# Kernel optimization log

Measured on AMD Instinct MI355X. Metric: run time of the kernel, lower is better.

## Reference

```python
import jax, jax.numpy as jnp
import numpy as np

DIM = 1024
HEADS = 8
DIM_HEAD = 64
INNER = HEADS * DIM_HEAD  # 512
SCALE = 8.0


def l2norm(t, eps=1e-12):
    # matches F.normalize(t, dim=-1)
    n = jnp.linalg.norm(t, axis=-1, keepdims=True)
    return t / jnp.maximum(n, eps)


def setup_inputs() -> dict:
    key = jax.random.key(0)
    ks = jax.random.split(key, 5)
    x = jax.random.normal(ks[0], (4, 2048, DIM), dtype=jnp.float32)
    # torch Linear weights are [out, in]; store transposed [in, out] for x @ W
    s = 1.0 / np.sqrt(DIM)
    Wq = jax.random.uniform(ks[1], (DIM, INNER), jnp.float32, -s, s)
    Wk = jax.random.uniform(ks[2], (DIM, INNER), jnp.float32, -s, s)
    Wv = jax.random.uniform(ks[3], (DIM, INNER), jnp.float32, -s, s)
    so = 1.0 / np.sqrt(INNER)
    Wo = jax.random.uniform(ks[4], (INNER, DIM), jnp.float32, -so, so)
    return {"x": x, "Wq": Wq, "Wk": Wk, "Wv": Wv, "Wo": Wo}


def reference(x, Wq, Wk, Wv, Wo):
    b, n, _ = x.shape
    def split_heads(t):
        return t.reshape(b, n, HEADS, DIM_HEAD).transpose(0, 2, 1, 3)  # b h n d
    q = split_heads(x @ Wq)
    k = split_heads(x @ Wk)
    v = split_heads(x @ Wv)
    # cosine-sim attention: l2-normalize q, k then fixed scale
    q = l2norm(q)
    k = l2norm(k)
    sim = jnp.einsum('bhid,bhjd->bhij', q, k) * SCALE
    causal_mask = jnp.triu(jnp.ones((n, n), dtype=bool), k=1)
    sim = jnp.where(causal_mask, jnp.finfo(sim.dtype).min, sim)
    attn = jax.nn.softmax(sim, axis=-1)
    o = jnp.einsum('bhij,bhjd->bhid', attn, v)
    o = o.transpose(0, 2, 1, 3).reshape(b, n, INNER)
    return o @ Wo
```

## Files before the change

kernel.cpp:

```cpp
#include <hip/hip_runtime.h>
#include <hip/hip_bf16.h>

typedef __attribute__((ext_vector_type(8))) __bf16 bf16x8;
typedef __attribute__((ext_vector_type(4))) __bf16 bf16x4;
typedef __attribute__((ext_vector_type(4))) float f32x4;

#define MFMA16(a, b, c) __builtin_amdgcn_mfma_f32_16x16x32_bf16(a, b, c, 0, 0, 0)

static __device__ __forceinline__ ushort f2b(float f) {
    __bf16 b = (__bf16)f;
    return __builtin_bit_cast(ushort, b);
}
static __device__ __forceinline__ bf16x8 cat44(bf16x4 a, bf16x4 b) {
    bf16x8 r;
    r[0] = a[0]; r[1] = a[1]; r[2] = a[2]; r[3] = a[3];
    r[4] = b[0]; r[5] = b[1]; r[6] = b[2]; r[7] = b[3];
    return r;
}
static __device__ __forceinline__ void gload_lds16(const ushort* g, ushort* l) {
    __builtin_amdgcn_global_load_lds(
        (const __attribute__((address_space(1))) unsigned int*)g,
        (__attribute__((address_space(3))) unsigned int*)l, 16, 0, 0);
}
static __device__ __forceinline__ float exp2_fast(float x) {
    float r;
    asm("v_exp_f32 %0, %1" : "=v"(r) : "v"(x));
    return r;
}

__global__ __launch_bounds__(256)
void prep_k(const float* __restrict__ x, ushort* __restrict__ xb,
            const float* __restrict__ Wq, const float* __restrict__ Wk,
            const float* __restrict__ Wv, const float* __restrict__ Wo,
            ushort* __restrict__ Wqkv, ushort* __restrict__ Wot) {
    const int bid = blockIdx.x;
    const int tid = threadIdx.x;
    if (bid < 8192) {
        int i = bid * 256 + tid;
        float4 v = reinterpret_cast<const float4*>(x)[i];
        ushort4 o;
        o.x = f2b(v.x); o.y = f2b(v.y); o.z = f2b(v.z); o.w = f2b(v.w);
        reinterpret_cast<ushort4*>(xb)[i] = o;
        return;
    }
    __shared__ ushort T[64][72];
    const int bb = bid - 8192;
    const int job = bb >> 7;
    const int t = bb & 127;
    const float* src; ushort* dst; int K, N;
    if (job == 0)      { src = Wq; dst = Wqkv;                       K = 1024; N = 512; }
    else if (job == 1) { src = Wk; dst = Wqkv + (size_t)512 * 1024;  K = 1024; N = 512; }
    else if (job == 2) { src = Wv; dst = Wqkv + (size_t)1024 * 1024; K = 1024; N = 512; }
    else               { src = Wo; dst = Wot;                        K = 512;  N = 1024; }
    const int tn = N >> 6;
    const int bk = t / tn, bn = t - bk * tn;
    const int k0 = bk * 64, n0 = bn * 64;
#pragma unroll
    for (int q = 0; q < 4; ++q) {
        const int lin = tid + 256 * q;
        const int kr = lin >> 4;
        const int n4 = (lin & 15) << 2;
        float4 v = *reinterpret_cast<const float4*>(&src[(size_t)(k0 + kr) * N + n0 + n4]);
        T[n4 + 0][kr] = f2b(v.x);
        T[n4 + 1][kr] = f2b(v.y);
        T[n4 + 2][kr] = f2b(v.z);
        T[n4 + 3][kr] = f2b(v.w);
    }
    __syncthreads();
#pragma unroll
    for (int s = 0; s < 2; ++s) {
        const int lin = tid + 256 * s;
        const int n = lin >> 3;
        const int kc = (lin & 7) << 3;
        ushort4 a, b;
        a.x = T[n][kc + 0]; a.y = T[n][kc + 1]; a.z = T[n][kc + 2]; a.w = T[n][kc + 3];
        b.x = T[n][kc + 4]; b.y = T[n][kc + 5]; b.z = T[n][kc + 6]; b.w = T[n][kc + 7];
        ushort* p = &dst[(size_t)(n0 + n) * K + k0 + kc];
        *reinterpret_cast<ushort4*>(p) = a;
        *reinterpret_cast<ushort4*>(p + 4) = b;
    }
}

template <int F32OUT, int ROUTE>
__global__ __launch_bounds__(256)
void gemm_tile_k(const ushort* __restrict__ A, const ushort* __restrict__ Bt,
                 void* __restrict__ C0, void* __restrict__ C1, void* __restrict__ C2,
                 int M, int N, int K, int nby) {
    __shared__ __align__(16) ushort As[128 * 64];
    __shared__ __align__(16) ushort Bs[128 * 64];
    const int tid = threadIdx.x;
    const int lane = tid & 63;
    const int w = tid >> 6;
    const int l15 = lane & 15, g = lane >> 4;
    const int wr = w >> 1, wc = w & 1;

    const int nwg = gridDim.x;
    const int cpx = nwg >> 3;
    const int bid = blockIdx.x;
    const int swz = (bid & 7) * cpx + (bid >> 3);
    const int bx = swz / nby, by = swz - bx * nby;
    const int rbase = bx * 128, cbase = by * 128;

    const int lr = lane >> 3;
    const int sc = (lane & 7) ^ lr;
    const ushort* Ap = A + (size_t)(rbase + 32 * w + lr) * K + sc * 8;
    const ushort* Bp = Bt + (size_t)(cbase + 32 * w + lr) * K + sc * 8;
    ushort* AsD = &As[(32 * w) * 64];
    ushort* BsD = &Bs[(32 * w) * 64];

    f32x4 acc[4][4];
#pragma unroll
    for (int m = 0; m < 4; ++m)
#pragma unroll
        for (int n = 0; n < 4; ++n) acc[m][n] = (f32x4){0, 0, 0, 0};

    const int nk = K >> 6;
    for (int kt = 0; kt < nk; ++kt) {
        const int k0 = kt << 6;
        if (kt) __syncthreads();
#pragma unroll
        for (int i = 0; i < 4; ++i) {
            gload_lds16(Ap + (size_t)(8 * i) * K + k0, AsD + (8 * i) * 64);
            gload_lds16(Bp + (size_t)(8 * i) * K + k0, BsD + (8 * i) * 64);
        }
        __syncthreads();
        bf16x8 af[4][2], bfr[4][2];
#pragma unroll
        for (int m = 0; m < 4; ++m) {
            const int row = 64 * wr + 16 * m + l15;
#pragma unroll
            for (int kh = 0; kh < 2; ++kh) {
                const int ch = (g + 4 * kh) ^ (l15 & 7);
                af[m][kh] = *reinterpret_cast<const bf16x8*>(&As[row * 64 + ch * 8]);
            }
        }
#pragma unroll
        for (int n = 0; n < 4; ++n) {
            const int row = 64 * wc + 16 * n + l15;
#pragma unroll
            for (int kh = 0; kh < 2; ++kh) {
                const int ch = (g + 4 * kh) ^ (l15 & 7);
                bfr[n][kh] = *reinterpret_cast<const bf16x8*>(&Bs[row * 64 + ch * 8]);
            }
        }
#pragma unroll
        for (int m = 0; m < 4; ++m)
#pragma unroll
            for (int n = 0; n < 4; ++n) {
                acc[m][n] = MFMA16(af[m][0], bfr[n][0], acc[m][n]);
                acc[m][n] = MFMA16(af[m][1], bfr[n][1], acc[m][n]);
            }
    }

    if (ROUTE) {
        const int col0 = cbase + 64 * wc;
        const int grp = col0 >> 9;
        const int co0 = col0 & 511;
        if (grp == 2) {
            const int h = co0 >> 6;
#pragma unroll
            for (int m = 0; m < 4; ++m) {
                const int row = rbase + 64 * wr + 16 * m + 4 * g;
                const int bb = row >> 11;
                const int tok = row & 2047;
#pragma unroll
                for (int n = 0; n < 4; ++n) {
                    const int d = 16 * n + l15;
                    bf16x4 wv;
#pragma unroll
                    for (int r = 0; r < 4; ++r) wv[r] = (__bf16)acc[m][n][r];
                    ushort* dst = (ushort*)C2 + (((size_t)(bb * 8 + h) * 64 + d) * 2048 + tok);
                    *reinterpret_cast<bf16x4*>(dst) = wv;
                }
            }
        } else {
            ushort* Cg = (ushort*)(grp == 0 ? C0 : C1);
#pragma unroll
            for (int m = 0; m < 4; ++m) {
                f32x4 ss = {0, 0, 0, 0};
#pragma unroll
                for (int n = 0; n < 4; ++n)
#pragma unroll
                    for (int r = 0; r < 4; ++r) ss[r] += acc[m][n][r] * acc[m][n][r];
#pragma unroll
                for (int r = 0; r < 4; ++r) {
                    float s = ss[r];
                    s += __shfl_xor(s, 1);
                    s += __shfl_xor(s, 2);
                    s += __shfl_xor(s, 4);
                    s += __shfl_xor(s, 8);
                    ss[r] = 1.0f / fmaxf(sqrtf(s), 1e-12f);
                }
                const int row = rbase + 64 * wr + 16 * m + 4 * g;
#pragma unroll
                for (int n = 0; n < 4; ++n) {
                    const int co = co0 + 16 * n + l15;
#pragma unroll
                    for (int r = 0; r < 4; ++r)
                        Cg[(size_t)(row + r) * 512 + co] = f2b(acc[m][n][r] * ss[r]);
                }
            }
        }
    } else {
#pragma unroll
        for (int m = 0; m < 4; ++m)
#pragma unroll
            for (int n = 0; n < 4; ++n) {
                const int row = rbase + 64 * wr + 16 * m + 4 * g;
                const int col = cbase + 64 * wc + 16 * n + l15;
                if (F32OUT) {
#pragma unroll
                    for (int r = 0; r < 4; ++r)
                        reinterpret_cast<float*>(C0)[(size_t)(row + r) * N + col] = acc[m][n][r];
                } else {
#pragma unroll
                    for (int r = 0; r < 4; ++r)
                        reinterpret_cast<ushort*>(C0)[(size_t)(row + r) * N + col] = f2b(acc[m][n][r]);
                }
            }
    }
}

__global__ __launch_bounds__(128, 2)
void flash_attn_k(const ushort* __restrict__ Q, const ushort* __restrict__ K,
                  const ushort* __restrict__ Vt, ushort* __restrict__ O) {
    __shared__ __align__(16) ushort Ks[64 * 64];
    __shared__ __align__(16) ushort Vs[64 * 64];
    const int tid = threadIdx.x;
    const int lane = tid & 63;
    const int wave = tid >> 6;
    const int l15 = lane & 15;
    const int g = lane >> 4;
    const int bh = blockIdx.x;
    const int b = bh >> 3, h = bh & 7;
    const int j = blockIdx.y;
    const int ytrue = (j < 16) ? j : 47 - j;
    const int wglob = ytrue * 2 + wave;
    const int c0 = wglob;
    const int c1 = 127 - wglob;
    const int q0 = c0 * 16 + l15;
    const int q1 = c1 * 16 + l15;
    const int nt0 = (c0 * 16 + 79) >> 6;
    const int nt1 = (c1 * 16 + 79) >> 6;
    const int ntb = ((127 - 2 * ytrue) * 16 + 79) >> 6;

    const float CEXP = 11.5415603f;

    const ushort* Qb = Q + (size_t)(b * 2048) * 512 + h * 64;
    const ushort* Kb = K + (size_t)(b * 2048) * 512 + h * 64;
    const ushort* Vb = Vt + (size_t)bh * 64 * 2048;

    const ushort* kSrc[4];
    const ushort* vSrc[4];
    ushort* kDst[4];
    ushort* vDst[4];
#pragma unroll
    for (int i = 0; i < 4; ++i) {
        const int s = tid + 128 * i;
        const int row = s >> 3;
        const int cc = s & 7;
        const int scc = cc ^ (row & 7);
        kSrc[i] = Kb + (size_t)row * 512 + scc * 8;
        vSrc[i] = Vb + (size_t)row * 2048 + scc * 8;
        const int base = (wave * 64 + 128 * i) * 8;
        kDst[i] = &Ks[base];
        vDst[i] = &Vs[base];
    }

    bf16x8 qf0[2], qf1[2];
#pragma unroll
    for (int kh = 0; kh < 2; ++kh) {
        qf0[kh] = *reinterpret_cast<const bf16x8*>(Qb + (size_t)q0 * 512 + 32 * kh + 8 * g);
        qf1[kh] = *reinterpret_cast<const bf16x8*>(Qb + (size_t)q1 * 512 + 32 * kh + 8 * g);
    }

    bf16x8 ones;
#pragma unroll
    for (int i = 0; i < 8; ++i) ones[i] = (__bf16)1.0f;

    f32x4 acc0[4], acc1[4];
#pragma unroll
    for (int d = 0; d < 4; ++d) {
        acc0[d] = (f32x4){0, 0, 0, 0};
        acc1[d] = (f32x4){0, 0, 0, 0};
    }
    f32x4 lac0 = {0, 0, 0, 0}, lac1 = {0, 0, 0, 0};

    for (int t = 0; t < ntb; ++t) {
        if (t) __syncthreads();
#pragma unroll
        for (int i = 0; i < 4; ++i) gload_lds16(kSrc[i] + (size_t)t * 32768, kDst[i]);
#pragma unroll
        for (int i = 0; i < 4; ++i) gload_lds16(vSrc[i] + t * 64, vDst[i]);
        __syncthreads();

        if (t >= nt1) continue;
        const bool act0 = (t < nt0);
        const bool mk0 = (t == nt0 - 1);
        const bool mk1 = (t == nt1 - 1);

        bf16x8 af[4][2];
#pragma unroll
        for (int jt = 0; jt < 4; ++jt)
#pragma unroll
            for (int kh = 0; kh < 2; ++kh) {
                const int row = jt * 16 + l15;
                const int chunk = (g + 4 * kh) ^ (row & 7);
                af[jt][kh] = *reinterpret_cast<const bf16x8*>(&Ks[row * 64 + chunk * 8]);
            }
        bf16x4 vf[4][2][2];
#pragma unroll
        for (int d = 0; d < 4; ++d)
#pragma unroll
            for (int kk = 0; kk < 2; ++kk)
#pragma unroll
                for (int th = 0; th < 2; ++th) {
                    const int dr = d * 16 + l15;
                    const int chunk = ((g >> 1) + 2 * th + 4 * kk) ^ (dr & 7);
                    vf[d][kk][th] = *reinterpret_cast<const bf16x4*>(
                        &Vs[dr * 64 + chunk * 8 + (g & 1) * 4]);
                }

        f32x4 s1[4], s0[4];
#pragma unroll
        for (int jt = 0; jt < 4; ++jt) {
            f32x4 z = {0, 0, 0, 0};
            z = MFMA16(af[jt][0], qf1[0], z);
            s1[jt] = MFMA16(af[jt][1], qf1[1], z);
        }
        if (act0) {
#pragma unroll
            for (int jt = 0; jt < 4; ++jt) {
                f32x4 z = {0, 0, 0, 0};
                z = MFMA16(af[jt][0], qf0[0], z);
                s0[jt] = MFMA16(af[jt][1], qf0[1], z);
            }
        }

        bf16x8 pt1[2];
#pragma unroll
        for (int jt = 0; jt < 4; ++jt) {
#pragma unroll
            for (int r = 0; r < 4; ++r) {
                float p = exp2_fast(fmaf(s1[jt][r], CEXP, -CEXP));
                if (mk1) {
                    int jj = t * 64 + jt * 16 + 4 * g + r;
                    p = (jj <= q1) ? p : 0.0f;
                }
                pt1[jt >> 1][(jt & 1) * 4 + r] = (__bf16)p;
            }
        }

        __builtin_amdgcn_s_setprio(1);
#pragma unroll
        for (int d = 0; d < 4; ++d) {
            bf16x8 v0 = cat44(vf[d][0][0], vf[d][0][1]);
            bf16x8 v1 = cat44(vf[d][1][0], vf[d][1][1]);
            acc1[d] = MFMA16(v0, pt1[0], acc1[d]);
            acc1[d] = MFMA16(v1, pt1[1], acc1[d]);
        }
        lac1 = MFMA16(ones, pt1[0], lac1);
        lac1 = MFMA16(ones, pt1[1], lac1);
        __builtin_amdgcn_s_setprio(0);

        if (act0) {
            bf16x8 pt0[2];
#pragma unroll
            for (int jt = 0; jt < 4; ++jt) {
#pragma unroll
                for (int r = 0; r < 4; ++r) {
                    float p = exp2_fast(fmaf(s0[jt][r], CEXP, -CEXP));
                    if (mk0) {
                        int jj = t * 64 + jt * 16 + 4 * g + r;
                        p = (jj <= q0) ? p : 0.0f;
                    }
                    pt0[jt >> 1][(jt & 1) * 4 + r] = (__bf16)p;
                }
            }
            __builtin_amdgcn_s_setprio(1);
#pragma unroll
            for (int d = 0; d < 4; ++d) {
                bf16x8 v0 = cat44(vf[d][0][0], vf[d][0][1]);
                bf16x8 v1 = cat44(vf[d][1][0], vf[d][1][1]);
                acc0[d] = MFMA16(v0, pt0[0], acc0[d]);
                acc0[d] = MFMA16(v1, pt0[1], acc0[d]);
            }
            lac0 = MFMA16(ones, pt0[0], lac0);
            lac0 = MFMA16(ones, pt0[1], lac0);
            __builtin_amdgcn_s_setprio(0);
        }
    }

    auto fin = [&](f32x4 (&acc)[4], float ls, int qr) {
        float inv = 1.0f / ls;
        ushort* Ob = O + (size_t)(b * 2048 + qr) * 512 + h * 64;
#pragma unroll
        for (int d = 0; d < 4; ++d) {
            bf16x4 w;
#pragma unroll
            for (int r = 0; r < 4; ++r) w[r] = (__bf16)(acc[d][r] * inv);
            *reinterpret_cast<bf16x4*>(Ob + d * 16 + 4 * g) = w;
        }
    };
    fin(acc1, lac1[0], q1);
    fin(acc0, lac0[0], q0);
}

extern "C" void kernel_launch(void* const* d_in, const int* in_sizes, int n_in,
                              void* d_out, int out_size, void* d_ws, size_t ws_size,
                              hipStream_t stream) {
    const float* x  = (const float*)d_in[0];
    const float* Wq = (const float*)d_in[1];
    const float* Wk = (const float*)d_in[2];
    const float* Wv = (const float*)d_in[3];
    const float* Wo = (const float*)d_in[4];
    float* out = (float*)d_out;

    char* ws = (char*)d_ws;
    ushort* xb  = (ushort*)ws; ws += (size_t)8192 * 1024 * 2;
    ushort* Wqt = (ushort*)ws; ws += (size_t)1536 * 1024 * 2;
    ushort* Wot = (ushort*)ws; ws += (size_t)1024 * 512 * 2;
    ushort* Qm  = (ushort*)ws; ws += (size_t)8192 * 512 * 2;
    ushort* Km  = (ushort*)ws; ws += (size_t)8192 * 512 * 2;
    ushort* Vtm = (ushort*)ws; ws += (size_t)8192 * 512 * 2;
    ushort* Om  = xb;

    prep_k<<<8704, 256, 0, stream>>>(x, xb, Wq, Wk, Wv, Wo, Wqt, Wot);

    gemm_tile_k<0, 1><<<768, 256, 0, stream>>>(xb, Wqt, Qm, Km, Vtm, 8192, 1536, 1024, 12);

    flash_attn_k<<<dim3(32, 32), 128, 0, stream>>>(Qm, Km, Vtm, Om);

    gemm_tile_k<1, 0><<<512, 256, 0, stream>>>(Om, Wot, out, nullptr, nullptr, 8192, 1024, 512, 8);
}
```

Before: 110.6 us.

## Use single-wave attention blocks with split K/V wait counts instead of barriers

The flash attention kernel changes from two-wave blocks sharing staged K/V tiles to one-wave blocks, which removes all __syncthreads and the per-block tile count padding needed when waves had different causal extents. Each wave now loads its own full 64x64 K and V tiles into LDS. A partial vmcnt wait lets QK^T and the exponentials start once K has arrived while the V loads are still in flight. The cost is twice the global-to-LDS traffic for K/V across blocks, and the loop relies on s_waitcnt lgkmcnt(0) at the end of each iteration to avoid overwriting LDS that is still being read, since there is no barrier.

Result: no change. 111.0 us (+0.4%).

```diff
diff --git a/kernel.cpp b/kernel.cpp
--- a/kernel.cpp
+++ b/kernel.cpp
@@ -221,28 +221,23 @@
     }
 }
 
-__global__ __launch_bounds__(128, 2)
+__global__ __launch_bounds__(64, 2)
 void flash_attn_k(const ushort* __restrict__ Q, const ushort* __restrict__ K,
                   const ushort* __restrict__ Vt, ushort* __restrict__ O) {
     __shared__ __align__(16) ushort Ks[64 * 64];
     __shared__ __align__(16) ushort Vs[64 * 64];
-    const int tid = threadIdx.x;
-    const int lane = tid & 63;
-    const int wave = tid >> 6;
+    const int lane = threadIdx.x & 63;
     const int l15 = lane & 15;
     const int g = lane >> 4;
     const int bh = blockIdx.x;
     const int b = bh >> 3, h = bh & 7;
-    const int j = blockIdx.y;
-    const int ytrue = (j < 16) ? j : 47 - j;
-    const int wglob = ytrue * 2 + wave;
+    const int wglob = blockIdx.y;
     const int c0 = wglob;
     const int c1 = 127 - wglob;
     const int q0 = c0 * 16 + l15;
     const int q1 = c1 * 16 + l15;
     const int nt0 = (c0 * 16 + 79) >> 6;
     const int nt1 = (c1 * 16 + 79) >> 6;
-    const int ntb = ((127 - 2 * ytrue) * 16 + 79) >> 6;
 
     const float CEXP = 11.5415603f;
 
@@ -250,22 +245,10 @@
     const ushort* Kb = K + (size_t)(b * 2048) * 512 + h * 64;
     const ushort* Vb = Vt + (size_t)bh * 64 * 2048;
 
-    const ushort* kSrc[4];
-    const ushort* vSrc[4];
-    ushort* kDst[4];
-    ushort* vDst[4];
-#pragma unroll
-    for (int i = 0; i < 4; ++i) {
-        const int s = tid + 128 * i;
-        const int row = s >> 3;
-        const int cc = s & 7;
-        const int scc = cc ^ (row & 7);
-        kSrc[i] = Kb + (size_t)row * 512 + scc * 8;
-        vSrc[i] = Vb + (size_t)row * 2048 + scc * 8;
-        const int base = (wave * 64 + 128 * i) * 8;
-        kDst[i] = &Ks[base];
-        vDst[i] = &Vs[base];
-    }
+    const int lr = lane >> 3;
+    const int scc = (lane & 7) ^ lr;
+    const ushort* kS = Kb + (size_t)lr * 512 + scc * 8;
+    const ushort* vS = Vb + (size_t)lr * 2048 + scc * 8;
 
     bf16x8 qf0[2], qf1[2];
 #pragma unroll
@@ -286,15 +269,16 @@
     }
     f32x4 lac0 = {0, 0, 0, 0}, lac1 = {0, 0, 0, 0};
 
-    for (int t = 0; t < ntb; ++t) {
-        if (t) __syncthreads();
-#pragma unroll
-        for (int i = 0; i < 4; ++i) gload_lds16(kSrc[i] + (size_t)t * 32768, kDst[i]);
-#pragma unroll
-        for (int i = 0; i < 4; ++i) gload_lds16(vSrc[i] + t * 64, vDst[i]);
-        __syncthreads();
-
-        if (t >= nt1) continue;
+    for (int t = 0; t < nt1; ++t) {
+#pragma unroll
+        for (int i = 0; i < 8; ++i)
+            gload_lds16(kS + (size_t)t * 32768 + (size_t)(8 * i) * 512, &Ks[(lane + 64 * i) * 8]);
+#pragma unroll
+        for (int i = 0; i < 8; ++i)
+            gload_lds16(vS + t * 64 + (size_t)(8 * i) * 2048, &Vs[(lane + 64 * i) * 8]);
+        asm volatile("s_waitcnt vmcnt(8)" ::: "memory");
+        __builtin_amdgcn_sched_barrier(0);
+
         const bool act0 = (t < nt0);
         const bool mk0 = (t == nt0 - 1);
         const bool mk1 = (t == nt1 - 1);
@@ -308,18 +292,6 @@
                 const int chunk = (g + 4 * kh) ^ (row & 7);
                 af[jt][kh] = *reinterpret_cast<const bf16x8*>(&Ks[row * 64 + chunk * 8]);
             }
-        bf16x4 vf[4][2][2];
-#pragma unroll
-        for (int d = 0; d < 4; ++d)
-#pragma unroll
-            for (int kk = 0; kk < 2; ++kk)
-#pragma unroll
-                for (int th = 0; th < 2; ++th) {
-                    const int dr = d * 16 + l15;
-                    const int chunk = ((g >> 1) + 2 * th + 4 * kk) ^ (dr & 7);
-                    vf[d][kk][th] = *reinterpret_cast<const bf16x4*>(
-                        &Vs[dr * 64 + chunk * 8 + (g & 1) * 4]);
-                }
 
         f32x4 s1[4], s0[4];
 #pragma unroll
@@ -337,7 +309,7 @@
             }
         }
 
-        bf16x8 pt1[2];
+        bf16x8 pt1[2], pt0[2];
 #pragma unroll
         for (int jt = 0; jt < 4; ++jt) {
 #pragma unroll
@@ -350,21 +322,7 @@
                 pt1[jt >> 1][(jt & 1) * 4 + r] = (__bf16)p;
             }
         }
-
-        __builtin_amdgcn_s_setprio(1);
-#pragma unroll
-        for (int d = 0; d < 4; ++d) {
-            bf16x8 v0 = cat44(vf[d][0][0], vf[d][0][1]);
-            bf16x8 v1 = cat44(vf[d][1][0], vf[d][1][1]);
-            acc1[d] = MFMA16(v0, pt1[0], acc1[d]);
-            acc1[d] = MFMA16(v1, pt1[1], acc1[d]);
-        }
-        lac1 = MFMA16(ones, pt1[0], lac1);
-        lac1 = MFMA16(ones, pt1[1], lac1);
-        __builtin_amdgcn_s_setprio(0);
-
         if (act0) {
-            bf16x8 pt0[2];
 #pragma unroll
             for (int jt = 0; jt < 4; ++jt) {
 #pragma unroll
@@ -377,7 +335,35 @@
                     pt0[jt >> 1][(jt & 1) * 4 + r] = (__bf16)p;
                 }
             }
-            __builtin_amdgcn_s_setprio(1);
+        }
+
+        asm volatile("s_waitcnt vmcnt(0)" ::: "memory");
+        __builtin_amdgcn_sched_barrier(0);
+
+        bf16x4 vf[4][2][2];
+#pragma unroll
+        for (int d = 0; d < 4; ++d)
+#pragma unroll
+            for (int kk = 0; kk < 2; ++kk)
+#pragma unroll
+                for (int th = 0; th < 2; ++th) {
+                    const int dr = d * 16 + l15;
+                    const int chunk = ((g >> 1) + 2 * th + 4 * kk) ^ (dr & 7);
+                    vf[d][kk][th] = *reinterpret_cast<const bf16x4*>(
+                        &Vs[dr * 64 + chunk * 8 + (g & 1) * 4]);
+                }
+
+        __builtin_amdgcn_s_setprio(1);
+#pragma unroll
+        for (int d = 0; d < 4; ++d) {
+            bf16x8 v0 = cat44(vf[d][0][0], vf[d][0][1]);
+            bf16x8 v1 = cat44(vf[d][1][0], vf[d][1][1]);
+            acc1[d] = MFMA16(v0, pt1[0], acc1[d]);
+            acc1[d] = MFMA16(v1, pt1[1], acc1[d]);
+        }
+        lac1 = MFMA16(ones, pt1[0], lac1);
+        lac1 = MFMA16(ones, pt1[1], lac1);
+        if (act0) {
 #pragma unroll
             for (int d = 0; d < 4; ++d) {
                 bf16x8 v0 = cat44(vf[d][0][0], vf[d][0][1]);
@@ -387,8 +373,11 @@
             }
             lac0 = MFMA16(ones, pt0[0], lac0);
             lac0 = MFMA16(ones, pt0[1], lac0);
-            __builtin_amdgcn_s_setprio(0);
-        }
+        }
+        __builtin_amdgcn_s_setprio(0);
+
+        asm volatile("s_waitcnt lgkmcnt(0)" ::: "memory");
+        __builtin_amdgcn_sched_barrier(0);
     }
 
     auto fin = [&](f32x4 (&acc)[4], float ls, int qr) {
@@ -429,7 +418,7 @@
 
     gemm_tile_k<0, 1><<<768, 256, 0, stream>>>(xb, Wqt, Qm, Km, Vtm, 8192, 1536, 1024, 12);
 
-    flash_attn_k<<<dim3(32, 32), 128, 0, stream>>>(Qm, Km, Vtm, Om);
+    flash_attn_k<<<dim3(32, 64), 64, 0, stream>>>(Qm, Km, Vtm, Om);
 
     gemm_tile_k<1, 0><<<512, 256, 0, stream>>>(Om, Wot, out, nullptr, nullptr, 8192, 1024, 512, 8);
 }
```
